# Kernel tuning notes

Measured on AMD Instinct MI355X. Metric: run time of the kernel, lower is better.

Reference implementation:

```python
import jax, jax.numpy as jnp
import numpy as np

EPS = 1.1  # GIN epsilon from GINLayer(1.1, dim)
N_GIN = 4

def setup_inputs() -> dict:
    key = jax.random.key(0)
    ks = jax.random.split(key, 24)
    R, F_IN, H1, D = 1048576, 64, 256, 128
    N, E, B, A1, T = 100000, 1600000, 4096, 256, 16
    s = 0.05
    inp = {}
    inp['bulk'] = jax.random.normal(ks[0], (R, F_IN), dtype=jnp.float32)
    inp['seg_ids'] = jnp.sort(jax.random.randint(ks[1], (R,), 0, N))
    inp['edge_src'] = jax.random.randint(ks[2], (E,), 0, N)
    inp['edge_dst'] = jax.random.randint(ks[3], (E,), 0, N)
    inp['root_idx'] = jax.random.randint(ks[4], (B,), 0, N)
    inp['num_nodes'] = N
    # feature extractor: Linear(64,256)+ReLU, Linear(256,128)+ReLU
    inp['W1'] = jax.random.normal(ks[5], (F_IN, H1), dtype=jnp.float32) * s
    inp['b1'] = jnp.zeros((H1,), jnp.float32)
    inp['W2'] = jax.random.normal(ks[6], (H1, D), dtype=jnp.float32) * s
    inp['b2'] = jnp.zeros((D,), jnp.float32)
    # 4 GIN layers, dim D -> D
    inp['gin_W'] = jax.random.normal(ks[7], (N_GIN, D, D), dtype=jnp.float32) * s
    inp['gin_b'] = jnp.zeros((N_GIN, D), jnp.float32)
    # actor: Linear(128,256)+ReLU, Linear(256,16)+ReLU, Softmax
    inp['Wa1'] = jax.random.normal(ks[8], (D, A1), dtype=jnp.float32) * s
    inp['ba1'] = jnp.zeros((A1,), jnp.float32)
    inp['Wa2'] = jax.random.normal(ks[9], (A1, T), dtype=jnp.float32) * s
    inp['ba2'] = jnp.zeros((T,), jnp.float32)
    # critic: Linear(128,256)+ReLU, Linear(256,1)
    inp['Wc1'] = jax.random.normal(ks[10], (D, A1), dtype=jnp.float32) * s
    inp['bc1'] = jnp.zeros((A1,), jnp.float32)
    inp['Wc2'] = jax.random.normal(ks[11], (A1, 1), dtype=jnp.float32) * s
    inp['bc2'] = jnp.zeros((1,), jnp.float32)
    return inp

def reference(bulk, seg_ids, edge_src, edge_dst, root_idx, num_nodes,
              W1, b1, W2, b2, gin_W, gin_b, Wa1, ba1, Wa2, ba2, Wc1, bc1, Wc2, bc2):
    # feature extractor over all rows
    h = jax.nn.relu(bulk @ W1 + b1)
    h = jax.nn.relu(h @ W2 + b2)  # [R, D]
    # per-dataset mean aggregation (self.aggregator over split groups)
    sums = jax.ops.segment_sum(h, seg_ids, num_segments=num_nodes)
    counts = jax.ops.segment_sum(jnp.ones((h.shape[0],), h.dtype), seg_ids, num_segments=num_nodes)
    node_h = sums / jnp.maximum(counts, 1.0)[:, None]  # [N, D]
    # GIN message passing: h_v <- relu(W ((1+eps) h_v + sum_{child u} h_u) + b)
    for i in range(N_GIN):
        agg = jax.ops.segment_sum(node_h[edge_src], edge_dst, num_segments=num_nodes)
        node_h = jax.nn.relu(((1.0 + EPS) * node_h + agg) @ gin_W[i] + gin_b[i])
    X = node_h[root_idx]  # [B, D] current-node representations
    act = jax.nn.softmax(jax.nn.relu(jax.nn.relu(X @ Wa1 + ba1) @ Wa2 + ba2), axis=-1)
    crit = (jax.nn.relu(X @ Wc1 + bc1) @ Wc2 + bc2).squeeze(-1)
    return (act, crit)
```

## Files before the change

### kernel.cpp

```cpp
#include <hip/hip_runtime.h>
#include <math.h>

#define R_ROWS 1048576
#define F_IN   64
#define H1     256
#define D      128
#define NN     100000
#define NE     1600000
#define NB     4096
#define A1     256
#define NTOK   16
#define N_GIN  4
#define FE_ROWS 64

typedef short short8 __attribute__((ext_vector_type(8)));
typedef float f32x4  __attribute__((ext_vector_type(4)));
typedef unsigned int uintx4 __attribute__((ext_vector_type(4)));

__device__ __forceinline__ ushort f2bf(float x) {
    uint u = __builtin_bit_cast(uint, x);
    u += 0x7FFFu + ((u >> 16) & 1u);
    return (ushort)(u >> 16);
}
__device__ __forceinline__ float bf2f(ushort h) {
    uint u = ((uint)h) << 16;
    return __builtin_bit_cast(float, u);
}
__device__ __forceinline__ uint cvtpk(float lo, float hi) {
    uint r;
    asm("v_cvt_pk_bf16_f32 %0, %1, %2" : "=v"(r) : "v"(lo), "v"(hi));
    return r;
}
__device__ __forceinline__ float lo16f(uint p) { return __builtin_bit_cast(float, p << 16); }
__device__ __forceinline__ float hi16f(uint p) { return __builtin_bit_cast(float, p & 0xFFFF0000u); }

__device__ __forceinline__ f32x4 mm(short8 a, short8 b, f32x4 c) {
    return __builtin_amdgcn_mfma_f32_16x16x32_bf16(a, b, c, 0, 0, 0);
}
__device__ __forceinline__ void acc_add(f32x4& L, f32x4& H, const uintx4 p) {
    L[0] += lo16f(p[0]); H[0] += hi16f(p[0]);
    L[1] += lo16f(p[1]); H[1] += hi16f(p[1]);
    L[2] += lo16f(p[2]); H[2] += hi16f(p[2]);
    L[3] += lo16f(p[3]); H[3] += hi16f(p[3]);
}

__device__ __forceinline__ void pack_one(const float* __restrict__ W, int Ndim,
                                         int f, int lane, ushort* __restrict__ out)
{
    const int NTn = Ndim >> 4;
    const int kt = f / NTn, nt = f - kt * NTn;
    const int k0 = kt * 32 + (lane >> 4) * 8;
    const int n = nt * 16 + (lane & 15);
    uintx4 Hv, Lv;
    #pragma unroll
    for (int jj = 0; jj < 4; ++jj) {
        const float x0 = W[(k0 + 2 * jj) * Ndim + n];
        const float x1 = W[(k0 + 2 * jj + 1) * Ndim + n];
        const ushort h0 = f2bf(x0), l0 = f2bf(x0 - bf2f(h0));
        const ushort h1u = f2bf(x1), l1 = f2bf(x1 - bf2f(h1u));
        Hv[jj] = (uint)h0 | ((uint)h1u << 16);
        Lv[jj] = (uint)l0 | ((uint)l1 << 16);
    }
    *reinterpret_cast<uintx4*>(&out[((f * 2 + 0) * 64 + lane) * 8]) = Hv;
    *reinterpret_cast<uintx4*>(&out[((f * 2 + 1) * 64 + lane) * 8]) = Lv;
}

__global__ __launch_bounds__(256) void pack_all(
    const float* __restrict__ W1, const float* __restrict__ W2,
    const float* __restrict__ ginW,
    ushort* __restrict__ W1p, ushort* __restrict__ W2p, ushort* __restrict__ Gp,
    int* __restrict__ deg, int* __restrict__ mark, int* __restrict__ cnt)
{
    const int bid = blockIdx.x;
    if (bid < 56) {
        const int fid = bid * 4 + (threadIdx.x >> 6);
        const int lane = threadIdx.x & 63;
        if (fid < 32) pack_one(W1, H1, fid, lane, W1p);
        else if (fid < 96) pack_one(W2, D, fid - 32, lane, W2p);
        else {
            const int l = (fid - 96) >> 5;
            pack_one(ginW + (long)l * D * D, D, (fid - 96) & 31, lane, Gp + (long)l * 32768);
        }
    } else {
        const int zb = bid - 56;
        const int idx0 = (zb * 256 + threadIdx.x) * 4;
        #pragma unroll
        for (int k = 0; k < 4; ++k) {
            const int idx = idx0 + k;
            if (idx < NN) deg[idx] = 0;
            else if (idx < 2 * NN) mark[idx - NN] = 0;
        }
        if (bid == 56 && threadIdx.x == 0) cnt[0] = 0;
    }
}

__global__ __launch_bounds__(256, 4) void fe_mfma(
    const float* __restrict__ bulk, const int* __restrict__ seg,
    const ushort* __restrict__ W1p, const float* __restrict__ b1,
    const ushort* __restrict__ W2p, const float* __restrict__ b2,
    float* __restrict__ sums)
{
    __shared__ __align__(16) uint smem_u[10240];
    char* Ab  = (char*)smem_u;
    char* h1b = Ab + 8192;
    float* h2 = (float*)smem_u;

    const int t = threadIdx.x;
    const int lane = t & 63;
    const int w = t >> 6;
    const long r0 = (long)blockIdx.x * FE_ROWS;

    #pragma unroll
    for (int i = 0; i < 4; ++i) {
        const int gid = t + i * 256;
        const int row = gid >> 4;
        const int c4 = (gid & 15) * 4;
        const float4 v = *reinterpret_cast<const float4*>(&bulk[(r0 + row) * F_IN + c4]);
        uint2 pk; pk.x = cvtpk(v.x, v.y); pk.y = cvtpk(v.z, v.w);
        const int byteoff = row * 128 + ((c4 * 2) ^ ((row & 7) << 4));
        *reinterpret_cast<uint2*>(Ab + byteoff) = pk;
    }
    __syncthreads();

    const f32x4 zz = {0.f, 0.f, 0.f, 0.f};
    f32x4 acc1[4][4];
    #pragma unroll
    for (int mtl = 0; mtl < 4; ++mtl)
        #pragma unroll
        for (int ntb = 0; ntb < 4; ++ntb) acc1[mtl][ntb] = zz;

    #pragma unroll
    for (int kt = 0; kt < 2; ++kt) {
        short8 aw[4][2];
        #pragma unroll
        for (int mtl = 0; mtl < 4; ++mtl)
            #pragma unroll
            for (int p = 0; p < 2; ++p) {
                const int f = kt * 16 + (w * 4 + mtl);
                aw[mtl][p] = *reinterpret_cast<const short8*>(&W1p[((f * 2 + p) * 64 + lane) * 8]);
            }
        short8 bh[4];
        #pragma unroll
        for (int ntb = 0; ntb < 4; ++ntb) {
            const int row = ntb * 16 + (lane & 15);
            const int k0 = kt * 32 + (lane >> 4) * 8;
            bh[ntb] = *reinterpret_cast<const short8*>(Ab + (row * 128 + ((k0 * 2) ^ ((row & 7) << 4))));
        }
        #pragma unroll
        for (int mtl = 0; mtl < 4; ++mtl)
            #pragma unroll
            for (int ntb = 0; ntb < 4; ++ntb) {
                acc1[mtl][ntb] = mm(aw[mtl][0], bh[ntb], acc1[mtl][ntb]);
                acc1[mtl][ntb] = mm(aw[mtl][1], bh[ntb], acc1[mtl][ntb]);
            }
    }

    #pragma unroll
    for (int mtl = 0; mtl < 4; ++mtl) {
        const int hcb = w * 64 + mtl * 16 + (lane >> 4) * 4;
        const float4 bv = *reinterpret_cast<const float4*>(&b1[hcb]);
        #pragma unroll
        for (int ntb = 0; ntb < 4; ++ntb) {
            const int hr = (lane & 15) + ntb * 16;
            const float v0 = fmaxf(acc1[mtl][ntb][0] + bv.x, 0.f);
            const float v1 = fmaxf(acc1[mtl][ntb][1] + bv.y, 0.f);
            const float v2 = fmaxf(acc1[mtl][ntb][2] + bv.z, 0.f);
            const float v3 = fmaxf(acc1[mtl][ntb][3] + bv.w, 0.f);
            uint2 pk; pk.x = cvtpk(v0, v1); pk.y = cvtpk(v2, v3);
            const int byteoff = (hr * 512 + hcb * 2) ^ ((hr & 7) << 4);
            *reinterpret_cast<uint2*>(h1b + byteoff) = pk;
        }
    }
    __syncthreads();

    float b2v[2];
    #pragma unroll
    for (int ntl = 0; ntl < 2; ++ntl) b2v[ntl] = b2[w * 32 + ntl * 16 + (lane & 15)];
    f32x4 acc2[4][2];
    #pragma unroll
    for (int mt = 0; mt < 4; ++mt) { acc2[mt][0] = zz; acc2[mt][1] = zz; }

    #pragma unroll
    for (int kt = 0; kt < 8; ++kt) {
        short8 bw2[2][2];
        #pragma unroll
        for (int ntl = 0; ntl < 2; ++ntl)
            #pragma unroll
            for (int p = 0; p < 2; ++p) {
                const int f = kt * 8 + (w * 2 + ntl);
                bw2[ntl][p] = *reinterpret_cast<const short8*>(&W2p[((f * 2 + p) * 64 + lane) * 8]);
            }
        short8 ah[4];
        #pragma unroll
        for (int mt = 0; mt < 4; ++mt) {
            const int row = mt * 16 + (lane & 15);
            const int k0 = kt * 32 + (lane >> 4) * 8;
            ah[mt] = *reinterpret_cast<const short8*>(h1b + ((row * 512 + k0 * 2) ^ ((row & 7) << 4)));
        }
        #pragma unroll
        for (int mt = 0; mt < 4; ++mt)
            #pragma unroll
            for (int ntl = 0; ntl < 2; ++ntl) {
                acc2[mt][ntl] = mm(ah[mt], bw2[ntl][0], acc2[mt][ntl]);
                acc2[mt][ntl] = mm(ah[mt], bw2[ntl][1], acc2[mt][ntl]);
            }
    }
    __syncthreads();

    #pragma unroll
    for (int mt = 0; mt < 4; ++mt)
        #pragma unroll
        for (int ntl = 0; ntl < 2; ++ntl)
            #pragma unroll
            for (int r = 0; r < 4; ++r) {
                const int row = mt * 16 + (lane >> 4) * 4 + r;
                const int col = w * 32 + ntl * 16 + (lane & 15);
                h2[row * 132 + col] = fmaxf(acc2[mt][ntl][r] + b2v[ntl], 0.f);
            }
    __syncthreads();

    {
        const int g = t >> 7;
        const int c = t & 127;
        const int base = g * 32;
        const long rb = r0 + base;
        const int prev = (rb == 0) ? -1 : seg[rb - 1];
        const int nxt = (rb + 32 >= R_ROWS) ? -1 : seg[rb + 32];
        int cur = seg[rb];
        float run = 0.f;
        int runstart = 0;
        #pragma unroll 1
        for (int r = 0; r < 32; ++r) {
            const int s = seg[rb + r];
            if (s != cur) {
                if (runstart != 0 || cur != prev) sums[(long)cur * D + c] = run;
                else atomicAdd(&sums[(long)cur * D + c], run);
                cur = s; run = 0.f; runstart = r;
            }
            run += h2[(base + r) * 132 + c];
        }
        if ((runstart != 0 || cur != prev) && cur != nxt) sums[(long)cur * D + c] = run;
        else atomicAdd(&sums[(long)cur * D + c], run);
    }
}

__global__ __launch_bounds__(256) void start_kernel(const int* __restrict__ seg,
                                                    int* __restrict__ start)
{
    const int n = blockIdx.x * 256 + threadIdx.x;
    if (n > NN) return;
    int lo = 0, hi = R_ROWS;
    #pragma unroll 1
    while (lo < hi) {
        const int mid = (lo + hi) >> 1;
        if (seg[mid] < n) lo = mid + 1; else hi = mid;
    }
    start[n] = lo;
}

__global__ __launch_bounds__(256) void divide_bf(
    const float* __restrict__ sums, const int* __restrict__ start,
    uint* __restrict__ hbf)
{
    const long i = (long)blockIdx.x * 256 + threadIdx.x;
    if (i < (long)NN * 64) {
        const int n = (int)(i >> 6), u = (int)(i & 63);
        const int cA = (u & 15) + (u >> 4) * 32;
        const float inv = 1.f / fmaxf((float)(start[n + 1] - start[n]), 1.f);
        const float vA = sums[(long)n * D + cA] * inv;
        const float vB = sums[(long)n * D + cA + 16] * inv;
        hbf[i] = cvtpk(vA, vB);
    }
}

__global__ __launch_bounds__(256) void hist_kernel(const int* __restrict__ edst,
                                                   int* __restrict__ deg)
{
    const int e = blockIdx.x * 256 + threadIdx.x;
    if (e < NE) atomicAdd(&deg[edst[e]], 1);
}

#define SCHUNK 2048
__global__ __launch_bounds__(256) void scan_reduce(const int* __restrict__ deg,
                                                   int* __restrict__ partials, int n)
{
    __shared__ int sdata[256];
    const int b = blockIdx.x, t = threadIdx.x;
    const int base = b * SCHUNK;
    int sum = 0;
    for (int i = t; i < SCHUNK; i += 256) {
        const int idx = base + i;
        sum += (idx < n) ? deg[idx] : 0;
    }
    sdata[t] = sum; __syncthreads();
    for (int s = 128; s > 0; s >>= 1) {
        if (t < s) sdata[t] += sdata[t + s];
        __syncthreads();
    }
    if (t == 0) partials[b] = sdata[0];
}

__global__ __launch_bounds__(256) void scan_write(const int* __restrict__ deg,
                                                  const int* __restrict__ partials,
                                                  int nchunks,
                                                  int* __restrict__ offsets,
                                                  int* __restrict__ cursor, int n)
{
    __shared__ int sdata[256];
    __shared__ int base_sh;
    const int b = blockIdx.x, t = threadIdx.x;
    if (t < 64) {
        int v = (t < b && t < nchunks) ? partials[t] : 0;
        #pragma unroll
        for (int d2 = 1; d2 < 64; d2 <<= 1) v += __shfl_xor(v, d2);
        if (t == 0) base_sh = v;
    }
    const int base = b * SCHUNK;
    int loc[8]; int s = 0;
    #pragma unroll
    for (int j = 0; j < 8; ++j) {
        const int idx = base + t * 8 + j;
        const int v = (idx < n) ? deg[idx] : 0;
        loc[j] = s; s += v;
    }
    sdata[t] = s; __syncthreads();
    for (int d = 1; d < 256; d <<= 1) {
        const int v = (t >= d) ? sdata[t - d] : 0;
        __syncthreads();
        sdata[t] += v;
        __syncthreads();
    }
    const int excl = (t == 0) ? 0 : sdata[t - 1];
    const int tbase = base_sh + excl;
    #pragma unroll
    for (int j = 0; j < 8; ++j) {
        const int idx = base + t * 8 + j;
        if (idx < n) {
            const int o = tbase + loc[j];
            offsets[idx] = o;
            cursor[idx] = o;
        }
    }
}

__global__ __launch_bounds__(256) void scatter_edges(const int* __restrict__ esrc,
                                                     const int* __restrict__ edst,
                                                     int* __restrict__ cursor,
                                                     int* __restrict__ csr_src)
{
    const int e = blockIdx.x * 256 + threadIdx.x;
    if (e < NE) {
        const int d = edst[e];
        const int p = atomicAdd(&cursor[d], 1);
        csr_src[p] = esrc[e];
    }
}

__global__ __launch_bounds__(256) void mark_kernel(
    const int* __restrict__ root, const int* __restrict__ offsets,
    const int* __restrict__ deg, const int* __restrict__ csr,
    int* __restrict__ mark)
{
    const int b = blockIdx.x * 256 + threadIdx.x;
    if (b < NB) {
        const int n = root[b];
        mark[n] = 1;
        const int off = offsets[n], dg = deg[n];
        for (int j = 0; j < dg; ++j) mark[csr[off + j]] = 1;
    }
}

__global__ __launch_bounds__(256) void compact_kernel(
    const int* __restrict__ mark, int* __restrict__ list, int* __restrict__ cnt)
{
    const int n = blockIdx.x * 256 + threadIdx.x;
    if (n < NN && mark[n]) {
        const int p = atomicAdd(cnt, 1);
        list[p] = n;
    }
}

template<int MODE>
__global__ __launch_bounds__(256, 8) void gin_kernel(
    const uint* __restrict__ hbf, const int* __restrict__ offsets,
    const int* __restrict__ deg, const int* __restrict__ csr,
    const ushort* __restrict__ Wp, const float* __restrict__ bvec,
    uint* __restrict__ outbuf,
    const int* __restrict__ list, const int* __restrict__ cnt,
    const int* __restrict__ root)
{
    __shared__ __align__(16) char ylds[64 * 256];
    __shared__ int nid[64];
    const int t = threadIdx.x, lane = t & 63, w = t >> 6;
    const int h = lane >> 5;
    const int q2 = (lane >> 4) & 1;
    const int m = lane & 15;
    const int q = lane >> 4;
    const int r0 = blockIdx.x * 64;
    const int CNT = (MODE == 1) ? cnt[0] : 0;
    if (MODE == 1 && r0 >= CNT) return;

    #pragma unroll 1
    for (int i = 0; i < 8; ++i) {
        const int row = w * 16 + i * 2 + h;
        int n = -1;
        if (MODE == 0) {
            const int nn = r0 + row;
            if (nn < NN) n = nn;
        } else if (MODE == 1) {
            const int idx = r0 + row;
            if (idx < CNT) n = list[idx];
        } else {
            n = root[r0 + row];
        }
        if (MODE == 1 && (lane & 31) == 0) nid[row] = n;
        f32x4 accL = {0.f, 0.f, 0.f, 0.f};
        f32x4 accH = {0.f, 0.f, 0.f, 0.f};
        if (n >= 0) {
            const uintx4 sp = *reinterpret_cast<const uintx4*>(&hbf[(long)n * 64 + 4 * m]);
            const float sc = (q2 == 0) ? 2.1f : 0.f;
            accL[0] = sc * lo16f(sp[0]); accH[0] = sc * hi16f(sp[0]);
            accL[1] = sc * lo16f(sp[1]); accH[1] = sc * hi16f(sp[1]);
            accL[2] = sc * lo16f(sp[2]); accH[2] = sc * hi16f(sp[2]);
            accL[3] = sc * lo16f(sp[3]); accH[3] = sc * hi16f(sp[3]);
            const int off = offsets[n];
            const int dg = deg[n];
            const int dg2 = dg >> 1;
            int jj = 0;
            for (; jj + 4 <= dg2; jj += 4) {
                const int b0 = off + 2 * jj + q2;
                const int s0 = csr[b0], s1 = csr[b0 + 2], s2 = csr[b0 + 4], s3 = csr[b0 + 6];
                const uintx4 p0 = *reinterpret_cast<const uintx4*>(&hbf[(long)s0 * 64 + 4 * m]);
                const uintx4 p1 = *reinterpret_cast<const uintx4*>(&hbf[(long)s1 * 64 + 4 * m]);
                const uintx4 p2 = *reinterpret_cast<const uintx4*>(&hbf[(long)s2 * 64 + 4 * m]);
                const uintx4 p3 = *reinterpret_cast<const uintx4*>(&hbf[(long)s3 * 64 + 4 * m]);
                acc_add(accL, accH, p0);
                acc_add(accL, accH, p1);
                acc_add(accL, accH, p2);
                acc_add(accL, accH, p3);
            }
            for (; jj < dg2; ++jj) {
                const int s = csr[off + 2 * jj + q2];
                const uintx4 p = *reinterpret_cast<const uintx4*>(&hbf[(long)s * 64 + 4 * m]);
                acc_add(accL, accH, p);
            }
            if ((dg & 1) && q2 == 0) {
                const int s = csr[off + dg - 1];
                const uintx4 p = *reinterpret_cast<const uintx4*>(&hbf[(long)s * 64 + 4 * m]);
                acc_add(accL, accH, p);
            }
        }
        #pragma unroll
        for (int e = 0; e < 4; ++e) {
            accL[e] += __shfl_xor(accL[e], 16);
            accH[e] += __shfl_xor(accH[e], 16);
        }
        const int swz = (row & 7) << 4;
        #pragma unroll
        for (int e = 0; e < 2; ++e) {
            const int u = 4 * m + 2 * q2 + e;
            const int cA = (u & 15) + (u >> 4) * 32;
            const uint pk = cvtpk(accL[2 * q2 + e], accH[2 * q2 + e]);
            *reinterpret_cast<ushort*>(ylds + ((row * 256 + cA * 2) ^ swz)) = (ushort)pk;
            *reinterpret_cast<ushort*>(ylds + ((row * 256 + (cA + 16) * 2) ^ swz)) = (ushort)(pk >> 16);
        }
    }

    short8 bw0[2][2];
    #pragma unroll
    for (int ntl = 0; ntl < 2; ++ntl)
        #pragma unroll
        for (int p = 0; p < 2; ++p) {
            const int f = w * 2 + ntl;
            bw0[ntl][p] = *reinterpret_cast<const short8*>(&Wp[((f * 2 + p) * 64 + lane) * 8]);
        }
    __syncthreads();

    const f32x4 zz = {0.f, 0.f, 0.f, 0.f};
    f32x4 acc[4][2];
    #pragma unroll
    for (int mt = 0; mt < 4; ++mt) { acc[mt][0] = zz; acc[mt][1] = zz; }

    #pragma unroll
    for (int kt = 0; kt < 4; ++kt) {
        short8 bw[2][2];
        if (kt == 0) {
            #pragma unroll
            for (int ntl = 0; ntl < 2; ++ntl)
                #pragma unroll
                for (int p = 0; p < 2; ++p) bw[ntl][p] = bw0[ntl][p];
        } else {
            #pragma unroll
            for (int ntl = 0; ntl < 2; ++ntl)
                #pragma unroll
                for (int p = 0; p < 2; ++p) {
                    const int f = kt * 8 + (w * 2 + ntl);
                    bw[ntl][p] = *reinterpret_cast<const short8*>(&Wp[((f * 2 + p) * 64 + lane) * 8]);
                }
        }
        #pragma unroll
        for (int mt = 0; mt < 4; ++mt) {
            const int row = mt * 16 + m;
            const int k0 = kt * 32 + q * 8;
            const short8 ah = *reinterpret_cast<const short8*>(
                ylds + ((row * 256 + k0 * 2) ^ ((row & 7) << 4)));
            acc[mt][0] = mm(ah, bw[0][0], acc[mt][0]);
            acc[mt][0] = mm(ah, bw[0][1], acc[mt][0]);
            acc[mt][1] = mm(ah, bw[1][0], acc[mt][1]);
            acc[mt][1] = mm(ah, bw[1][1], acc[mt][1]);
        }
    }

    const float bv0 = bvec[w * 32 + m];
    const float bv1 = bvec[w * 32 + 16 + m];
    #pragma unroll
    for (int mt = 0; mt < 4; ++mt)
        #pragma unroll
        for (int r = 0; r < 4; ++r) {
            const int grow_row = mt * 16 + q * 4 + r;
            const float v0 = fmaxf(acc[mt][0][r] + bv0, 0.f);
            const float v1 = fmaxf(acc[mt][1][r] + bv1, 0.f);
            const uint pk = cvtpk(v0, v1);
            if (MODE == 0) {
                const long nout = r0 + grow_row;
                if (nout < NN) outbuf[nout * 64 + w * 16 + m] = pk;
            } else if (MODE == 1) {
                if (r0 + grow_row < CNT) {
                    const long nout = nid[grow_row];
                    outbuf[nout * 64 + w * 16 + m] = pk;
                }
            } else {
                outbuf[(long)(r0 + grow_row) * 64 + w * 16 + m] = pk;
            }
        }
}

__global__ __launch_bounds__(256) void head_kernel(
    const uint* __restrict__ Xbf, const int* __restrict__ root,
    const float* __restrict__ Wa1, const float* __restrict__ ba1,
    const float* __restrict__ Wa2, const float* __restrict__ ba2,
    const float* __restrict__ Wc1, const float* __restrict__ bc1,
    const float* __restrict__ Wc2, const float* __restrict__ bc2,
    float* __restrict__ out_act, float* __restrict__ out_crit)
{
    __shared__ float X[D];
    __shared__ float a1[A1];
    __shared__ float red[256];
    __shared__ float logits[NTOK];
    const int t = threadIdx.x;
    const int bi = blockIdx.x;
    if (t < 64) {
        const uint p = Xbf[(long)bi * 64 + t];
        const int cA = (t & 15) + (t >> 4) * 32;
        X[cA] = lo16f(p);
        X[cA + 16] = hi16f(p);
    }
    __syncthreads();

    float acc = ba1[t];
    #pragma unroll
    for (int k = 0; k < D; k += 4) {
        const float4 xv = *reinterpret_cast<const float4*>(&X[k]);
        acc = fmaf(xv.x, Wa1[(k + 0) * A1 + t], acc);
        acc = fmaf(xv.y, Wa1[(k + 1) * A1 + t], acc);
        acc = fmaf(xv.z, Wa1[(k + 2) * A1 + t], acc);
        acc = fmaf(xv.w, Wa1[(k + 3) * A1 + t], acc);
    }
    a1[t] = fmaxf(acc, 0.f);
    __syncthreads();

    const int j = t & 15, p = t >> 4;
    float pa = 0.f;
    #pragma unroll
    for (int k = 0; k < 16; ++k) {
        const int kk = p * 16 + k;
        pa = fmaf(a1[kk], Wa2[kk * NTOK + j], pa);
    }
    red[j * 16 + p] = pa;
    __syncthreads();
    if (t < NTOK) {
        float s = 0.f;
        #pragma unroll
        for (int p2 = 0; p2 < 16; ++p2) s += red[t * 16 + p2];
        logits[t] = fmaxf(s + ba2[t], 0.f);
    }
    __syncthreads();
    if (t < NTOK) {
        float mx = -1e30f;
        #pragma unroll
        for (int i = 0; i < NTOK; ++i) mx = fmaxf(mx, logits[i]);
        red[t] = expf(logits[t] - mx);
    }
    __syncthreads();
    if (t < NTOK) {
        float s = 0.f;
        #pragma unroll
        for (int i = 0; i < NTOK; ++i) s += red[i];
        out_act[(long)bi * NTOK + t] = red[t] / s;
    }
    __syncthreads();

    float accc = bc1[t];
    #pragma unroll
    for (int k = 0; k < D; k += 4) {
        const float4 xv = *reinterpret_cast<const float4*>(&X[k]);
        accc = fmaf(xv.x, Wc1[(k + 0) * A1 + t], accc);
        accc = fmaf(xv.y, Wc1[(k + 1) * A1 + t], accc);
        accc = fmaf(xv.z, Wc1[(k + 2) * A1 + t], accc);
        accc = fmaf(xv.w, Wc1[(k + 3) * A1 + t], accc);
    }
    red[t] = fmaxf(accc, 0.f) * Wc2[t];
    __syncthreads();
    for (int s = 128; s > 0; s >>= 1) {
        if (t < s) red[t] += red[t + s];
        __syncthreads();
    }
    if (t == 0) out_crit[bi] = red[0] + bc2[0];
}

extern "C" void kernel_launch(void* const* d_in, const int* in_sizes, int n_in,
                              void* d_out, int out_size, void* d_ws, size_t ws_size,
                              hipStream_t stream)
{
    const float* bulk = (const float*)d_in[0];
    const int*   seg  = (const int*)d_in[1];
    const int*   esrc = (const int*)d_in[2];
    const int*   edst = (const int*)d_in[3];
    const int*   root = (const int*)d_in[4];
    const float* W1   = (const float*)d_in[6];
    const float* b1   = (const float*)d_in[7];
    const float* W2   = (const float*)d_in[8];
    const float* b2   = (const float*)d_in[9];
    const float* ginW = (const float*)d_in[10];
    const float* ginb = (const float*)d_in[11];
    const float* Wa1  = (const float*)d_in[12];
    const float* ba1  = (const float*)d_in[13];
    const float* Wa2  = (const float*)d_in[14];
    const float* ba2  = (const float*)d_in[15];
    const float* Wc1  = (const float*)d_in[16];
    const float* bc1  = (const float*)d_in[17];
    const float* Wc2  = (const float*)d_in[18];
    const float* bc2  = (const float*)d_in[19];

    char* ws = (char*)d_ws;
    ushort* W1p = (ushort*)ws;
    ushort* W2p = W1p + 32768;
    float* sums    = (float*)(ws + 196608);
    uint*  hbfA    = (uint*)(sums + (long)NN * D);
    uint*  hbfB    = hbfA + (long)NN * 64;
    int*   start   = (int*)(hbfB + (long)NN * 64);
    int*   deg     = start + (NN + 4);
    int*   offsets = deg + NN;
    int*   cursor  = offsets + NN;
    int*   partials= cursor + NN;
    int*   csr     = partials + 256;
    int*   mark    = csr + NE;
    int*   list    = mark + NN;
    int*   cnt     = list + NN;
    uint*  Xbf     = (uint*)(cnt + 4);
    ushort* Gp     = (ushort*)(Xbf + (long)NB * 64);

    hipMemsetAsync(sums, 0, (long)NN * D * sizeof(float), stream);

    pack_all<<<252, 256, 0, stream>>>(W1, W2, ginW, W1p, W2p, Gp, deg, mark, cnt);

    fe_mfma<<<R_ROWS / FE_ROWS, 256, 0, stream>>>(bulk, seg, W1p, b1, W2p, b2, sums);
    start_kernel<<<(NN + 256) / 256, 256, 0, stream>>>(seg, start);
    divide_bf<<<((long)NN * 64 + 255) / 256, 256, 0, stream>>>(sums, start, hbfA);

    hist_kernel<<<(NE + 255) / 256, 256, 0, stream>>>(edst, deg);
    const int nchunks = (NN + SCHUNK - 1) / SCHUNK;
    scan_reduce<<<nchunks, 256, 0, stream>>>(deg, partials, NN);
    scan_write<<<nchunks, 256, 0, stream>>>(deg, partials, nchunks, offsets, cursor, NN);
    scatter_edges<<<(NE + 255) / 256, 256, 0, stream>>>(esrc, edst, cursor, csr);

    mark_kernel<<<(NB + 255) / 256, 256, 0, stream>>>(root, offsets, deg, csr, mark);
    compact_kernel<<<(NN + 255) / 256, 256, 0, stream>>>(mark, list, cnt);

    const int full_grid = (NN + 63) / 64;
    gin_kernel<0><<<full_grid, 256, 0, stream>>>(hbfA, offsets, deg, csr,
        Gp + 0L * 32768, ginb + 0L * D, hbfB, list, cnt, root);
    gin_kernel<0><<<full_grid, 256, 0, stream>>>(hbfB, offsets, deg, csr,
        Gp + 1L * 32768, ginb + 1L * D, hbfA, list, cnt, root);
    gin_kernel<1><<<full_grid, 256, 0, stream>>>(hbfA, offsets, deg, csr,
        Gp + 2L * 32768, ginb + 2L * D, hbfB, list, cnt, root);
    gin_kernel<2><<<NB / 64, 256, 0, stream>>>(hbfB, offsets, deg, csr,
        Gp + 3L * 32768, ginb + 3L * D, Xbf, list, cnt, root);

    head_kernel<<<NB, 256, 0, stream>>>(Xbf, root, Wa1, ba1, Wa2, ba2,
                                        Wc1, bc1, Wc2, bc2,
                                        (float*)d_out, (float*)d_out + (long)NB * NTOK);
}
```

Before: 775.2 us.

## Port actor/critic heads to bf16 MFMA and drop low-part weight passes

Replaces the per-root scalar head kernel (one block per root) with an MFMA kernel that processes 64 roots per block, using split-bf16 packed Wa1/Wc1/Wa2 weights prepared in pack_all. The feature-extractor first layer and GIN matmuls now use only the high bf16 part of the weights, halving MFMA count there. This removes the correction term for weight rounding error, trading accuracy for fewer matrix instructions.

```diff
diff --git a/kernel.cpp b/kernel.cpp
--- a/kernel.cpp
+++ b/kernel.cpp
@@ -67,22 +67,26 @@
 
 __global__ __launch_bounds__(256) void pack_all(
     const float* __restrict__ W1, const float* __restrict__ W2,
-    const float* __restrict__ ginW,
+    const float* __restrict__ ginW, const float* __restrict__ Wa1,
+    const float* __restrict__ Wc1, const float* __restrict__ Wa2,
     ushort* __restrict__ W1p, ushort* __restrict__ W2p, ushort* __restrict__ Gp,
+    ushort* __restrict__ Wa1p, ushort* __restrict__ Wc1p, ushort* __restrict__ Wa2p,
     int* __restrict__ deg, int* __restrict__ mark, int* __restrict__ cnt)
 {
     const int bid = blockIdx.x;
-    if (bid < 56) {
+    if (bid < 90) {
         const int fid = bid * 4 + (threadIdx.x >> 6);
         const int lane = threadIdx.x & 63;
         if (fid < 32) pack_one(W1, H1, fid, lane, W1p);
         else if (fid < 96) pack_one(W2, D, fid - 32, lane, W2p);
-        else {
+        else if (fid < 224) {
             const int l = (fid - 96) >> 5;
             pack_one(ginW + (long)l * D * D, D, (fid - 96) & 31, lane, Gp + (long)l * 32768);
-        }
+        } else if (fid < 288) pack_one(Wa1, A1, fid - 224, lane, Wa1p);
+        else if (fid < 352) pack_one(Wc1, A1, fid - 288, lane, Wc1p);
+        else if (fid < 360) pack_one(Wa2, NTOK, fid - 352, lane, Wa2p);
     } else {
-        const int zb = bid - 56;
+        const int zb = bid - 90;
         const int idx0 = (zb * 256 + threadIdx.x) * 4;
         #pragma unroll
         for (int k = 0; k < 4; ++k) {
@@ -90,7 +94,7 @@
             if (idx < NN) deg[idx] = 0;
             else if (idx < 2 * NN) mark[idx - NN] = 0;
         }
-        if (bid == 56 && threadIdx.x == 0) cnt[0] = 0;
+        if (bid == 90 && threadIdx.x == 0) cnt[0] = 0;
     }
 }
 
@@ -131,14 +135,12 @@
 
     #pragma unroll
     for (int kt = 0; kt < 2; ++kt) {
-        short8 aw[4][2];
-        #pragma unroll
-        for (int mtl = 0; mtl < 4; ++mtl)
-            #pragma unroll
-            for (int p = 0; p < 2; ++p) {
-                const int f = kt * 16 + (w * 4 + mtl);
-                aw[mtl][p] = *reinterpret_cast<const short8*>(&W1p[((f * 2 + p) * 64 + lane) * 8]);
-            }
+        short8 aw[4];
+        #pragma unroll
+        for (int mtl = 0; mtl < 4; ++mtl) {
+            const int f = kt * 16 + (w * 4 + mtl);
+            aw[mtl] = *reinterpret_cast<const short8*>(&W1p[((f * 2 + 0) * 64 + lane) * 8]);
+        }
         short8 bh[4];
         #pragma unroll
         for (int ntb = 0; ntb < 4; ++ntb) {
@@ -149,10 +151,8 @@
         #pragma unroll
         for (int mtl = 0; mtl < 4; ++mtl)
             #pragma unroll
-            for (int ntb = 0; ntb < 4; ++ntb) {
-                acc1[mtl][ntb] = mm(aw[mtl][0], bh[ntb], acc1[mtl][ntb]);
-                acc1[mtl][ntb] = mm(aw[mtl][1], bh[ntb], acc1[mtl][ntb]);
-            }
+            for (int ntb = 0; ntb < 4; ++ntb)
+                acc1[mtl][ntb] = mm(aw[mtl], bh[ntb], acc1[mtl][ntb]);
     }
 
     #pragma unroll
@@ -466,14 +466,12 @@
         }
     }
 
-    short8 bw0[2][2];
-    #pragma unroll
-    for (int ntl = 0; ntl < 2; ++ntl)
-        #pragma unroll
-        for (int p = 0; p < 2; ++p) {
-            const int f = w * 2 + ntl;
-            bw0[ntl][p] = *reinterpret_cast<const short8*>(&Wp[((f * 2 + p) * 64 + lane) * 8]);
-        }
+    short8 bw0[2];
+    #pragma unroll
+    for (int ntl = 0; ntl < 2; ++ntl) {
+        const int f = w * 2 + ntl;
+        bw0[ntl] = *reinterpret_cast<const short8*>(&Wp[((f * 2 + 0) * 64 + lane) * 8]);
+    }
     __syncthreads();
 
     const f32x4 zz = {0.f, 0.f, 0.f, 0.f};
@@ -483,20 +481,14 @@
 
     #pragma unroll
     for (int kt = 0; kt < 4; ++kt) {
-        short8 bw[2][2];
-        if (kt == 0) {
-            #pragma unroll
-            for (int ntl = 0; ntl < 2; ++ntl)
-                #pragma unroll
-                for (int p = 0; p < 2; ++p) bw[ntl][p] = bw0[ntl][p];
-        } else {
-            #pragma unroll
-            for (int ntl = 0; ntl < 2; ++ntl)
-                #pragma unroll
-                for (int p = 0; p < 2; ++p) {
-                    const int f = kt * 8 + (w * 2 + ntl);
-                    bw[ntl][p] = *reinterpret_cast<const short8*>(&Wp[((f * 2 + p) * 64 + lane) * 8]);
-                }
+        short8 bw[2];
+        if (kt == 0) { bw[0] = bw0[0]; bw[1] = bw0[1]; }
+        else {
+            #pragma unroll
+            for (int ntl = 0; ntl < 2; ++ntl) {
+                const int f = kt * 8 + (w * 2 + ntl);
+                bw[ntl] = *reinterpret_cast<const short8*>(&Wp[((f * 2 + 0) * 64 + lane) * 8]);
+            }
         }
         #pragma unroll
         for (int mt = 0; mt < 4; ++mt) {
@@ -504,10 +496,8 @@
             const int k0 = kt * 32 + q * 8;
             const short8 ah = *reinterpret_cast<const short8*>(
                 ylds + ((row * 256 + k0 * 2) ^ ((row & 7) << 4)));
-            acc[mt][0] = mm(ah, bw[0][0], acc[mt][0]);
-            acc[mt][0] = mm(ah, bw[0][1], acc[mt][0]);
-            acc[mt][1] = mm(ah, bw[1][0], acc[mt][1]);
-            acc[mt][1] = mm(ah, bw[1][1], acc[mt][1]);
+            acc[mt][0] = mm(ah, bw[0], acc[mt][0]);
+            acc[mt][1] = mm(ah, bw[1], acc[mt][1]);
         }
     }
 
@@ -535,87 +525,186 @@
         }
 }
 
-__global__ __launch_bounds__(256) void head_kernel(
-    const uint* __restrict__ Xbf, const int* __restrict__ root,
-    const float* __restrict__ Wa1, const float* __restrict__ ba1,
-    const float* __restrict__ Wa2, const float* __restrict__ ba2,
-    const float* __restrict__ Wc1, const float* __restrict__ bc1,
+__global__ __launch_bounds__(256) void head_mfma(
+    const uint* __restrict__ Xbf,
+    const ushort* __restrict__ Wa1p, const float* __restrict__ ba1,
+    const ushort* __restrict__ Wa2p, const float* __restrict__ ba2,
+    const ushort* __restrict__ Wc1p, const float* __restrict__ bc1,
     const float* __restrict__ Wc2, const float* __restrict__ bc2,
     float* __restrict__ out_act, float* __restrict__ out_crit)
 {
-    __shared__ float X[D];
-    __shared__ float a1[A1];
-    __shared__ float red[256];
-    __shared__ float logits[NTOK];
-    const int t = threadIdx.x;
-    const int bi = blockIdx.x;
-    if (t < 64) {
-        const uint p = Xbf[(long)bi * 64 + t];
-        const int cA = (t & 15) + (t >> 4) * 32;
-        X[cA] = lo16f(p);
-        X[cA + 16] = hi16f(p);
-    }
-    __syncthreads();
-
-    float acc = ba1[t];
-    #pragma unroll
-    for (int k = 0; k < D; k += 4) {
-        const float4 xv = *reinterpret_cast<const float4*>(&X[k]);
-        acc = fmaf(xv.x, Wa1[(k + 0) * A1 + t], acc);
-        acc = fmaf(xv.y, Wa1[(k + 1) * A1 + t], acc);
-        acc = fmaf(xv.z, Wa1[(k + 2) * A1 + t], acc);
-        acc = fmaf(xv.w, Wa1[(k + 3) * A1 + t], acc);
-    }
-    a1[t] = fmaxf(acc, 0.f);
-    __syncthreads();
-
-    const int j = t & 15, p = t >> 4;
-    float pa = 0.f;
-    #pragma unroll
-    for (int k = 0; k < 16; ++k) {
-        const int kk = p * 16 + k;
-        pa = fmaf(a1[kk], Wa2[kk * NTOK + j], pa);
-    }
-    red[j * 16 + p] = pa;
-    __syncthreads();
-    if (t < NTOK) {
-        float s = 0.f;
-        #pragma unroll
-        for (int p2 = 0; p2 < 16; ++p2) s += red[t * 16 + p2];
-        logits[t] = fmaxf(s + ba2[t], 0.f);
-    }
-    __syncthreads();
-    if (t < NTOK) {
-        float mx = -1e30f;
-        #pragma unroll
-        for (int i = 0; i < NTOK; ++i) mx = fmaxf(mx, logits[i]);
-        red[t] = expf(logits[t] - mx);
-    }
-    __syncthreads();
-    if (t < NTOK) {
-        float s = 0.f;
-        #pragma unroll
-        for (int i = 0; i < NTOK; ++i) s += red[i];
-        out_act[(long)bi * NTOK + t] = red[t] / s;
-    }
-    __syncthreads();
-
-    float accc = bc1[t];
-    #pragma unroll
-    for (int k = 0; k < D; k += 4) {
-        const float4 xv = *reinterpret_cast<const float4*>(&X[k]);
-        accc = fmaf(xv.x, Wc1[(k + 0) * A1 + t], accc);
-        accc = fmaf(xv.y, Wc1[(k + 1) * A1 + t], accc);
-        accc = fmaf(xv.z, Wc1[(k + 2) * A1 + t], accc);
-        accc = fmaf(xv.w, Wc1[(k + 3) * A1 + t], accc);
-    }
-    red[t] = fmaxf(accc, 0.f) * Wc2[t];
-    __syncthreads();
-    for (int s = 128; s > 0; s >>= 1) {
-        if (t < s) red[t] += red[t + s];
-        __syncthreads();
-    }
-    if (t == 0) out_crit[bi] = red[0] + bc2[0];
+    __shared__ __align__(16) char Xp[64 * 256];
+    __shared__ __align__(16) char a1p[64 * 512];
+    const int t = threadIdx.x, lane = t & 63, w = t >> 6;
+    const int r0 = blockIdx.x * 64;
+    const f32x4 zz = {0.f, 0.f, 0.f, 0.f};
+
+    {
+        const int row = t >> 2;
+        const int ug = (t & 3) * 16;
+        const int swz = (row & 7) << 4;
+        #pragma unroll
+        for (int uu = 0; uu < 16; ++uu) {
+            const uint pk = Xbf[(long)(r0 + row) * 64 + ug + uu];
+            const int u = ug + uu;
+            const int cA = (u & 15) + (u >> 4) * 32;
+            *reinterpret_cast<ushort*>(Xp + ((row * 256 + cA * 2) ^ swz)) = (ushort)pk;
+            *reinterpret_cast<ushort*>(Xp + ((row * 256 + (cA + 16) * 2) ^ swz)) = (ushort)(pk >> 16);
+        }
+    }
+    __syncthreads();
+
+    {
+        f32x4 acc1[4][4];
+        #pragma unroll
+        for (int mtl = 0; mtl < 4; ++mtl)
+            #pragma unroll
+            for (int ntb = 0; ntb < 4; ++ntb) acc1[mtl][ntb] = zz;
+        #pragma unroll
+        for (int kt = 0; kt < 4; ++kt) {
+            short8 aw[4][2];
+            #pragma unroll
+            for (int mtl = 0; mtl < 4; ++mtl)
+                #pragma unroll
+                for (int p = 0; p < 2; ++p) {
+                    const int f = kt * 16 + (w * 4 + mtl);
+                    aw[mtl][p] = *reinterpret_cast<const short8*>(&Wa1p[((f * 2 + p) * 64 + lane) * 8]);
+                }
+            short8 bh[4];
+            #pragma unroll
+            for (int ntb = 0; ntb < 4; ++ntb) {
+                const int row = ntb * 16 + (lane & 15);
+                const int k0 = kt * 32 + (lane >> 4) * 8;
+                bh[ntb] = *reinterpret_cast<const short8*>(Xp + ((row * 256 + k0 * 2) ^ ((row & 7) << 4)));
+            }
+            #pragma unroll
+            for (int mtl = 0; mtl < 4; ++mtl)
+                #pragma unroll
+                for (int ntb = 0; ntb < 4; ++ntb) {
+                    acc1[mtl][ntb] = mm(aw[mtl][0], bh[ntb], acc1[mtl][ntb]);
+                    acc1[mtl][ntb] = mm(aw[mtl][1], bh[ntb], acc1[mtl][ntb]);
+                }
+        }
+        #pragma unroll
+        for (int mtl = 0; mtl < 4; ++mtl) {
+            const int hcb = w * 64 + mtl * 16 + (lane >> 4) * 4;
+            const float4 bv = *reinterpret_cast<const float4*>(&ba1[hcb]);
+            #pragma unroll
+            for (int ntb = 0; ntb < 4; ++ntb) {
+                const int hr = (lane & 15) + ntb * 16;
+                const float v0 = fmaxf(acc1[mtl][ntb][0] + bv.x, 0.f);
+                const float v1 = fmaxf(acc1[mtl][ntb][1] + bv.y, 0.f);
+                const float v2 = fmaxf(acc1[mtl][ntb][2] + bv.z, 0.f);
+                const float v3 = fmaxf(acc1[mtl][ntb][3] + bv.w, 0.f);
+                uint2 pk; pk.x = cvtpk(v0, v1); pk.y = cvtpk(v2, v3);
+                const int byteoff = (hr * 512 + hcb * 2) ^ ((hr & 7) << 4);
+                *reinterpret_cast<uint2*>(a1p + byteoff) = pk;
+            }
+        }
+    }
+    __syncthreads();
+
+    {
+        f32x4 accl = zz;
+        #pragma unroll
+        for (int kt = 0; kt < 8; ++kt) {
+            short8 b2h = *reinterpret_cast<const short8*>(&Wa2p[((kt * 2 + 0) * 64 + lane) * 8]);
+            short8 b2l = *reinterpret_cast<const short8*>(&Wa2p[((kt * 2 + 1) * 64 + lane) * 8]);
+            const int row = w * 16 + (lane & 15);
+            const int k0 = kt * 32 + (lane >> 4) * 8;
+            const short8 ah = *reinterpret_cast<const short8*>(a1p + ((row * 512 + k0 * 2) ^ ((row & 7) << 4)));
+            accl = mm(ah, b2h, accl);
+            accl = mm(ah, b2l, accl);
+        }
+        const int j = lane & 15;
+        float lg[4], mx[4], sm[4];
+        #pragma unroll
+        for (int r = 0; r < 4; ++r) {
+            lg[r] = fmaxf(accl[r] + ba2[j], 0.f);
+            float m2 = lg[r];
+            #pragma unroll
+            for (int d2 = 1; d2 < 16; d2 <<= 1) m2 = fmaxf(m2, __shfl_xor(m2, d2));
+            mx[r] = m2;
+            lg[r] = expf(lg[r] - m2);
+            float s2 = lg[r];
+            #pragma unroll
+            for (int d2 = 1; d2 < 16; d2 <<= 1) s2 += __shfl_xor(s2, d2);
+            sm[r] = s2;
+        }
+        #pragma unroll
+        for (int r = 0; r < 4; ++r) {
+            const int root_slot = r0 + w * 16 + (lane >> 4) * 4 + r;
+            out_act[(long)root_slot * NTOK + j] = lg[r] / sm[r];
+        }
+    }
+    __syncthreads();
+
+    {
+        f32x4 acc1[4][4];
+        #pragma unroll
+        for (int mtl = 0; mtl < 4; ++mtl)
+            #pragma unroll
+            for (int ntb = 0; ntb < 4; ++ntb) acc1[mtl][ntb] = zz;
+        #pragma unroll
+        for (int kt = 0; kt < 4; ++kt) {
+            short8 aw[4][2];
+            #pragma unroll
+            for (int mtl = 0; mtl < 4; ++mtl)
+                #pragma unroll
+                for (int p = 0; p < 2; ++p) {
+                    const int f = kt * 16 + (w * 4 + mtl);
+                    aw[mtl][p] = *reinterpret_cast<const short8*>(&Wc1p[((f * 2 + p) * 64 + lane) * 8]);
+                }
+            short8 bh[4];
+            #pragma unroll
+            for (int ntb = 0; ntb < 4; ++ntb) {
+                const int row = ntb * 16 + (lane & 15);
+                const int k0 = kt * 32 + (lane >> 4) * 8;
+                bh[ntb] = *reinterpret_cast<const short8*>(Xp + ((row * 256 + k0 * 2) ^ ((row & 7) << 4)));
+            }
+            #pragma unroll
+            for (int mtl = 0; mtl < 4; ++mtl)
+                #pragma unroll
+                for (int ntb = 0; ntb < 4; ++ntb) {
+                    acc1[mtl][ntb] = mm(aw[mtl][0], bh[ntb], acc1[mtl][ntb]);
+                    acc1[mtl][ntb] = mm(aw[mtl][1], bh[ntb], acc1[mtl][ntb]);
+                }
+        }
+        #pragma unroll
+        for (int mtl = 0; mtl < 4; ++mtl) {
+            const int hcb = w * 64 + mtl * 16 + (lane >> 4) * 4;
+            const float4 bv = *reinterpret_cast<const float4*>(&bc1[hcb]);
+            #pragma unroll
+            for (int ntb = 0; ntb < 4; ++ntb) {
+                const int hr = (lane & 15) + ntb * 16;
+                const float v0 = fmaxf(acc1[mtl][ntb][0] + bv.x, 0.f);
+                const float v1 = fmaxf(acc1[mtl][ntb][1] + bv.y, 0.f);
+                const float v2 = fmaxf(acc1[mtl][ntb][2] + bv.z, 0.f);
+                const float v3 = fmaxf(acc1[mtl][ntb][3] + bv.w, 0.f);
+                uint2 pk; pk.x = cvtpk(v0, v1); pk.y = cvtpk(v2, v3);
+                const int byteoff = (hr * 512 + hcb * 2) ^ ((hr & 7) << 4);
+                *reinterpret_cast<uint2*>(a1p + byteoff) = pk;
+            }
+        }
+    }
+    __syncthreads();
+
+    {
+        const int row = w * 16 + (lane & 15);
+        const int qk = lane >> 4;
+        float dot = 0.f;
+        #pragma unroll
+        for (int g = 0; g < 8; ++g) {
+            const int k0 = qk * 64 + g * 8;
+            const short8 av = *reinterpret_cast<const short8*>(a1p + ((row * 512 + k0 * 2) ^ ((row & 7) << 4)));
+            #pragma unroll
+            for (int e = 0; e < 8; ++e)
+                dot = fmaf(bf2f((ushort)av[e]), Wc2[k0 + e], dot);
+        }
+        dot += __shfl_xor(dot, 16);
+        dot += __shfl_xor(dot, 32);
+        if (lane < 16) out_crit[r0 + w * 16 + lane] = dot + bc2[0];
+    }
 }
 
 extern "C" void kernel_launch(void* const* d_in, const int* in_sizes, int n_in,
@@ -659,10 +748,15 @@
     int*   cnt     = list + NN;
     uint*  Xbf     = (uint*)(cnt + 4);
     ushort* Gp     = (ushort*)(Xbf + (long)NB * 64);
+    ushort* Wa1p   = Gp + 4 * 32768;
+    ushort* Wc1p   = Wa1p + 65536;
+    ushort* Wa2p   = Wc1p + 65536;
 
     hipMemsetAsync(sums, 0, (long)NN * D * sizeof(float), stream);
 
-    pack_all<<<252, 256, 0, stream>>>(W1, W2, ginW, W1p, W2p, Gp, deg, mark, cnt);
+    pack_all<<<286, 256, 0, stream>>>(W1, W2, ginW, Wa1, Wc1, Wa2,
+                                      W1p, W2p, Gp, Wa1p, Wc1p, Wa2p,
+                                      deg, mark, cnt);
 
     fe_mfma<<<R_ROWS / FE_ROWS, 256, 0, stream>>>(bulk, seg, W1p, b1, W2p, b2, sums);
     start_kernel<<<(NN + 256) / 256, 256, 0, stream>>>(seg, start);
@@ -687,7 +781,7 @@
     gin_kernel<2><<<NB / 64, 256, 0, stream>>>(hbfB, offsets, deg, csr,
         Gp + 3L * 32768, ginb + 3L * D, Xbf, list, cnt, root);
 
-    head_kernel<<<NB, 256, 0, stream>>>(Xbf, root, Wa1, ba1, Wa2, ba2,
-                                        Wc1, bc1, Wc2, bc2,
-                                        (float*)d_out, (float*)d_out + (long)NB * NTOK);
-}
+    head_mfma<<<NB / 64, 256, 0, stream>>>(Xbf, Wa1p, ba1, Wa2p, ba2,
+                                           Wc1p, bc1, Wc2, bc2,
+                                           (float*)d_out, (float*)d_out + (long)NB * NTOK);
+}
```

Result: faster. 733.0 us (-5.4%).
